# Kernel optimization log

Measured on AMD Instinct MI355X. Metric: run time of the kernel, lower is better.

Reference implementation:

```python
import jax, jax.numpy as jnp
import numpy as np

B, D = 8, 256
MEM, CW, R, K, KL = 131072, 64, 4, 4, 4
C = R * K + 2 * KL + 1  # 25 visible cells
DELTA = 0.005
EPS = 1e-6
TIMESTEP = 1.0  # first step after reset


def _gather(x, idx):
    # x: (b,m) or (b,m,w); idx: (b,k)
    if x.ndim == 2:
        return jnp.take_along_axis(x, idx, axis=1)
    e = jnp.broadcast_to(idx[:, :, None], idx.shape + (x.shape[-1],))
    return jnp.take_along_axis(x, e, axis=1)


def _fwd(xi, memory, visible_memory, link_matrix, rev_link_matrix, precedence,
         read_weights, write_weights, usage,
         W_rq, b_rq, W_wv, b_wv, W_ig, b_ig, W_wg, b_wg,
         read_positions):
    b = xi.shape[0]
    bidx = jnp.arange(b)[:, None]

    # interface transforms (independent linears)
    read_query = (xi @ W_rq + b_rq).reshape(b, R, CW)      # (b,r,w)
    write_vector = (xi @ W_wv + b_wv).reshape(b, 1, CW)    # (b,1,w)
    ig = jax.nn.sigmoid(xi @ W_ig + b_ig)                  # (b,c)
    wg = jax.nn.sigmoid(xi @ W_wg + b_wg)                  # (b,1)

    # ------------------ write ------------------
    rw_vis = _gather(read_weights, read_positions)         # (b,c)
    ww_vis = _gather(write_weights, read_positions)        # (b,c)

    # usage update + least-used indicator over visible cells
    u = (rw_vis + ww_vis > DELTA).astype(memory.dtype)
    rel = _gather(usage, read_positions)
    I_min = (rel == jnp.min(rel, axis=-1, keepdims=True)).astype(memory.dtype)
    rel_new = (TIMESTEP - rel) * u + rel * (1.0 - u)
    usage = usage.at[bidx, read_positions].set(rel_new)

    # interpolated write weights over visible cells
    ww_new = wg * (ig * rw_vis + (1.0 - ig) * I_min)       # (b,c)
    write_weights = write_weights.at[bidx, read_positions].set(ww_new)

    # erase + write into visible memory, scatter back into sparse memory
    visible_memory = visible_memory * (1.0 - I_min[:, :, None]) + ww_new[:, :, None] * write_vector
    memory = memory.at[bidx, read_positions].set(visible_memory)

    # link matrix / reverse link matrix update
    trp = read_positions[:, R * K:R * K + 2 * KL]          # temporal positions (b,2KL)
    Ieye = jnp.eye(MEM, 2 * KL, dtype=memory.dtype)[None]  # eye(m,k) mask as in torch code
    prec_dense = jnp.zeros_like(write_weights).at[bidx, trp].set(precedence)  # (b,m)
    tww = _gather(write_weights, trp)                      # (b,2KL)
    link_matrix = ((1.0 - write_weights[:, :, None]) * link_matrix
                   + write_weights[:, :, None] * precedence[:, None, :]) * Ieye
    rev_link_matrix = ((1.0 - tww[:, None, :]) * rev_link_matrix
                       + tww[:, None, :] * prec_dense[:, :, None]) * Ieye

    # precedence update and least-used cell (argmin usage)
    precedence = (1.0 - jnp.sum(tww, axis=-1, keepdims=True)) * precedence + tww
    least_used = jax.lax.top_k(-usage, 1)[1]               # (b,1)

    # ------------------ read ------------------
    trw = _gather(read_weights, trp)                       # (b,2KL)
    fwd_w = jnp.einsum('bmk,bk->bm', link_matrix, trw)     # forward weighting
    bwd_w = jnp.einsum('bmk,bk->bm', rev_link_matrix, trw) # backward weighting

    # exact L2 k-NN over full memory (dense surrogate for the FAISS search)
    mem_sq = jnp.sum(memory * memory, axis=-1)             # (b,m)
    dots = jnp.einsum('brw,bmw->brm', read_query, memory)  # (b,r,m)
    knn = jax.lax.top_k(2.0 * dots - mem_sq[:, None, :], K)[1].reshape(b, R * K)

    fp = jax.lax.top_k(fwd_w, KL)[1]
    bp = jax.lax.top_k(bwd_w, KL)[1]
    lum = jnp.full((b, 1), C + 1, dtype=knn.dtype)         # timestep <= mem_size branch
    max_length = least_used[0, 0]                          # mem_limit_reached == False
    positions = jnp.clip(
        jnp.concatenate([knn, fp.astype(knn.dtype), bp.astype(knn.dtype), lum], axis=1),
        0, max_length)                                     # (b,c)

    visible = _gather(memory, positions)                   # (b,c,w)
    kq = read_query / (jnp.linalg.norm(read_query, axis=-1, keepdims=True) + EPS)
    vn = visible / (jnp.linalg.norm(visible, axis=-1, keepdims=True) + EPS)
    sim = jnp.einsum('brw,bcw->brc', kq, vn)               # cosine similarity
    rw_c = jax.nn.softmax(sim, axis=-1)                    # (b,r,c)
    read_vectors = jnp.einsum('brc,bcw->brw', rw_c, visible)
    return read_vectors


def setup_inputs() -> dict:
    key = jax.random.key(0)
    ks = jax.random.split(key, 16)
    inp = {}
    inp['xi'] = jax.random.normal(ks[0], (B, D), jnp.float32)
    inp['memory'] = jax.random.normal(ks[1], (B, MEM, CW), jnp.float32)
    inp['visible_memory'] = jax.random.normal(ks[2], (B, C, CW), jnp.float32)
    inp['link_matrix'] = 0.1 * jax.random.uniform(ks[3], (B, MEM, 2 * KL), jnp.float32)
    inp['rev_link_matrix'] = 0.1 * jax.random.uniform(ks[4], (B, MEM, 2 * KL), jnp.float32)
    inp['precedence'] = 0.1 * jax.random.uniform(ks[5], (B, 2 * KL), jnp.float32)
    inp['read_weights'] = 0.01 * jax.random.uniform(ks[6], (B, MEM), jnp.float32)
    inp['write_weights'] = 0.01 * jax.random.uniform(ks[7], (B, MEM), jnp.float32)
    usage = 0.5 + 0.5 * jax.random.uniform(ks[8], (B, MEM), jnp.float32)
    inp['usage'] = usage.at[:, MEM - 1].set(0.0)  # argmin lands at m-1 so the clamp is a no-op
    inp['least_used_mem'] = jnp.full((B, 1), MEM // 2, jnp.int32)
    inp['read_positions'] = jax.random.randint(ks[9], (B, C), 0, MEM)

    def lin(k, fi, fo):
        s = (6.0 / fi) ** 0.5  # kaiming-uniform-like
        return jax.random.uniform(k, (fi, fo), jnp.float32, -s, s)
    inp['W_rq'] = lin(ks[10], D, R * CW); inp['b_rq'] = jnp.zeros((R * CW,), jnp.float32)
    inp['W_wv'] = lin(ks[11], D, CW);     inp['b_wv'] = jnp.zeros((CW,), jnp.float32)
    inp['W_ig'] = lin(ks[12], D, C);      inp['b_ig'] = jnp.zeros((C,), jnp.float32)
    inp['W_wg'] = lin(ks[13], D, 1);      inp['b_wg'] = jnp.zeros((1,), jnp.float32)
    return inp


def reference(xi, memory, visible_memory, link_matrix, rev_link_matrix, precedence,
              read_weights, write_weights, usage, least_used_mem, read_positions,
              W_rq, b_rq, W_wv, b_wv, W_ig, b_ig, W_wg, b_wg):
    # least_used_mem is overwritten inside write() (argmin of updated usage) before use
    return _fwd(xi, memory, visible_memory, link_matrix, rev_link_matrix, precedence,
                read_weights, write_weights, usage,
                W_rq, b_rq, W_wv, b_wv, W_ig, b_ig, W_wg, b_wg,
                read_positions)
```

## Files before the change

### kernel.cpp

```cpp
#include <hip/hip_runtime.h>
#include <math.h>

#define BN 8
#define DDIM 256
#define MEMN 131072
#define CWN 64
#define RN 4
#define CN 25
#define DELTA_C 0.005f
#define EPS_C 1e-6f
#define RPB 1024
#define NBLK (MEMN / RPB)
#define NEG_INF (-3.402823466e38f)
#define IMAX 0x7fffffff
#define UPD_STRIDE 32


__device__ inline void wave_reduce_max(float& v, int& i, int& t) {
#pragma unroll
  for (int off = 32; off; off >>= 1) {
    float ov = __shfl_down(v, off);
    int oi = __shfl_down(i, off);
    int ot = __shfl_down(t, off);
    if (ov > v || (ov == v && oi < i)) { v = ov; i = oi; t = ot; }
  }
}

__device__ inline void block_argmax256(int tid, float v, int i, int t,
                                       float& rv, int& ri, int& rt) {
  __shared__ float sv[4];
  __shared__ int si[4], st[4];
  __shared__ float bv;
  __shared__ int bi, bt;
  wave_reduce_max(v, i, t);
  if ((tid & 63) == 0) { int w = tid >> 6; sv[w] = v; si[w] = i; st[w] = t; }
  __syncthreads();
  if (tid == 0) {
    float xv = sv[0]; int xi = si[0], xt = st[0];
#pragma unroll
    for (int w = 1; w < 4; w++)
      if (sv[w] > xv || (sv[w] == xv && si[w] < xi)) { xv = sv[w]; xi = si[w]; xt = st[w]; }
    bv = xv; bi = xi; bt = xt;
  }
  __syncthreads();
  rv = bv; ri = bi; rt = bt;
  __syncthreads();
}

__device__ inline void top4_of8(const float* v8, int* out4) {
  float val[12]; int idx[12]; bool used[12];
#pragma unroll
  for (int i = 0; i < 12; i++) { val[i] = (i < 8) ? v8[i] : 0.f; idx[i] = i; used[i] = false; }
  for (int r = 0; r < 4; r++) {
    int best = -1;
    for (int i = 0; i < 12; i++) {
      if (used[i]) continue;
      if (best < 0 || val[i] > val[best]) best = i;
    }
    used[best] = true;
    out4[r] = idx[best];
  }
}

__global__ __launch_bounds__(256) void k1_heads(
    const float* __restrict__ xi,
    const float* __restrict__ Wrq, const float* __restrict__ brq,
    const float* __restrict__ Wwv, const float* __restrict__ bwv,
    const float* __restrict__ Wig, const float* __restrict__ big,
    const float* __restrict__ Wwg, const float* __restrict__ bwg,
    float* rq, float* wv, float* ig, float* wg) {
  int b = blockIdx.x, tid = threadIdx.x;
  __shared__ float x[DDIM];
  x[tid] = xi[b * DDIM + tid];
  __syncthreads();
  {
    float s = brq[tid];
#pragma unroll 8
    for (int d = 0; d < DDIM; d++) s = fmaf(x[d], Wrq[d * 256 + tid], s);
    rq[b * 256 + tid] = s;
  }
  if (tid < 64) {
    float s = bwv[tid];
#pragma unroll 8
    for (int d = 0; d < DDIM; d++) s = fmaf(x[d], Wwv[d * 64 + tid], s);
    wv[b * 64 + tid] = s;
  } else if (tid < 64 + CN) {
    int o = tid - 64;
    float s = big[o];
#pragma unroll 8
    for (int d = 0; d < DDIM; d++) s = fmaf(x[d], Wig[d * CN + o], s);
    ig[b * CN + o] = 1.f / (1.f + expf(-s));
  } else if (tid == 64 + CN) {
    float s = bwg[0];
#pragma unroll 8
    for (int d = 0; d < DDIM; d++) s = fmaf(x[d], Wwg[d], s);
    wg[b] = 1.f / (1.f + expf(-s));
  }
}

__global__ __launch_bounds__(256) void k2_state(
    const float* __restrict__ vm, const float* __restrict__ prec,
    const float* __restrict__ rw, const float* __restrict__ wwg,
    const float* __restrict__ usage,
    const float* __restrict__ lm, const float* __restrict__ rlm,
    const int* __restrict__ rp,
    const float* __restrict__ wv, const float* __restrict__ ig,
    const float* __restrict__ wg, int* fp, int* bp,
    int* upd_pos, float* upd_rel, float* upd_mem) {
  int b = blockIdx.x, tid = threadIdx.x;
  __shared__ int pos[CN];
  __shared__ float s_rw[CN], s_ww[CN], s_rel[CN], s_relnew[CN], s_imin[CN], s_wwnew[CN];
  __shared__ int s_guard[CN];
  __shared__ float minrel;
  __shared__ float fwd8[8], bwd8[8];

  if (tid < CN) {
    int p = rp[b * CN + tid];
    pos[tid] = p;
    s_rw[tid] = rw[(size_t)b * MEMN + p];
    s_ww[tid] = wwg[(size_t)b * MEMN + p];
    s_rel[tid] = usage[(size_t)b * MEMN + p];
  }
  __syncthreads();
  if (tid == 0) {
    float m = s_rel[0];
    for (int j = 1; j < CN; j++) m = fminf(m, s_rel[j]);
    minrel = m;
  }
  __syncthreads();
  if (tid < CN) {
    float u = (s_rw[tid] + s_ww[tid] > DELTA_C) ? 1.f : 0.f;
    float im = (s_rel[tid] == minrel) ? 1.f : 0.f;
    s_imin[tid] = im;
    s_relnew[tid] = u * (1.f - s_rel[tid]) + (1.f - u) * s_rel[tid];
    float igv = ig[b * CN + tid];
    s_wwnew[tid] = wg[b] * (igv * s_rw[tid] + (1.f - igv) * im);
    int g = 1;
    for (int j = tid + 1; j < CN; j++)
      if (pos[j] == pos[tid]) { g = 0; break; }
    s_guard[tid] = g;
  }
  __syncthreads();
  if (tid < CN) {
    upd_pos[b * UPD_STRIDE + tid] = s_guard[tid] ? pos[tid] : -1;
    upd_rel[b * UPD_STRIDE + tid] = s_relnew[tid];
  }
  for (int it = 0; it < 7; it++) {
    int j = it * 4 + (tid >> 6);
    int lane = tid & 63;
    if (j < CN && s_guard[j]) {
      float v = vm[((size_t)b * CN + j) * 64 + lane] * (1.f - s_imin[j]) +
                s_wwnew[j] * wv[b * 64 + lane];
      upd_mem[((size_t)b * CN + j) * 64 + lane] = v;
    }
  }
  __syncthreads();
  if (tid < 8) {
    int m = tid;
    int trp_m = pos[16 + m];
    float tww = 0.f;
    for (int j = CN - 1; j >= 0; j--)
      if (pos[j] == trp_m) { tww = s_wwnew[j]; break; }
    float trw = rw[(size_t)b * MEMN + trp_m];
    float wwu;
    {
      int found = -1;
      for (int j = CN - 1; j >= 0; j--)
        if (pos[j] == m) { found = j; break; }
      wwu = (found >= 0) ? s_wwnew[found] : wwg[(size_t)b * MEMN + m];
    }
    float lmd = (1.f - wwu) * lm[((size_t)b * MEMN + m) * 8 + m] + wwu * prec[b * 8 + m];
    float pd = 0.f;
    for (int k = 7; k >= 0; k--)
      if (pos[16 + k] == m) { pd = prec[b * 8 + k]; break; }
    float rld = (1.f - tww) * rlm[((size_t)b * MEMN + m) * 8 + m] + tww * pd;
    fwd8[m] = lmd * trw;
    bwd8[m] = rld * trw;
  }
  __syncthreads();
  if (tid == 0) top4_of8(fwd8, &fp[b * 4]);
  if (tid == 1) top4_of8(bwd8, &bp[b * 4]);
}

__global__ __launch_bounds__(256) void k3_scan(
    const float* __restrict__ memory, const float* __restrict__ usage,
    const float* __restrict__ rq,
    const int* __restrict__ upd_pos, const float* __restrict__ upd_rel,
    const float* __restrict__ upd_mem,
    float* blk_sv, int* blk_si, float* blk_uv, int* blk_ui) {
  int tid = threadIdx.x;
  int b = blockIdx.x / NBLK;
  int blk = blockIdx.x % NBLK;
  int base = blk * RPB;
  int wave = tid >> 6, lane = tid & 63;
  int sub = lane & 15;
  int grp = lane >> 4;

  __shared__ int s_lcnt;
  __shared__ int s_lpos[CN], s_lj[CN];
  __shared__ float s_lrel[CN];
  if (tid == 0) s_lcnt = 0;
  __syncthreads();
  if (tid < CN) {
    int p = upd_pos[b * UPD_STRIDE + tid];
    if (p >= base && p < base + RPB) {
      int k = atomicAdd(&s_lcnt, 1);
      s_lpos[k] = p;
      s_lj[k] = tid;
      s_lrel[k] = upd_rel[b * UPD_STRIDE + tid];
    }
  }
  __syncthreads();
  int lcnt = s_lcnt;
  const float4* upd4 = (const float4*)upd_mem;

  const float4* q4 = (const float4*)(rq + b * 256);
  float4 qf0 = q4[0 * 16 + sub];
  float4 qf1 = q4[1 * 16 + sub];
  float4 qf2 = q4[2 * 16 + sub];
  float4 qf3 = q4[3 * 16 + sub];

  float tv0 = NEG_INF, tv1 = NEG_INF, tv2 = NEG_INF, tv3 = NEG_INF;
  int ti0 = IMAX, ti1 = IMAX, ti2 = IMAX, ti3 = IMAX;

  int rowbase = base + wave * 256;
  const float4* mp = (const float4*)memory;
  size_t lanebase = ((size_t)b * MEMN + rowbase) * 16 + (size_t)grp * 16 + sub;

#pragma unroll 4
  for (int it = 0; it < 64; it++) {
    int m = rowbase + it * 4 + grp;
    float4 x = mp[lanebase + (size_t)it * 64];
    if (lcnt) {
      for (int k = 0; k < lcnt; k++)
        if (m == s_lpos[k])
          x = upd4[((size_t)b * CN + s_lj[k]) * 16 + sub];
    }
    float d0 = fmaf(x.x, qf0.x, fmaf(x.y, qf0.y, fmaf(x.z, qf0.z, x.w * qf0.w)));
    float d1 = fmaf(x.x, qf1.x, fmaf(x.y, qf1.y, fmaf(x.z, qf1.z, x.w * qf1.w)));
    float d2 = fmaf(x.x, qf2.x, fmaf(x.y, qf2.y, fmaf(x.z, qf2.z, x.w * qf2.w)));
    float d3 = fmaf(x.x, qf3.x, fmaf(x.y, qf3.y, fmaf(x.z, qf3.z, x.w * qf3.w)));
    float sq = fmaf(x.x, x.x, fmaf(x.y, x.y, fmaf(x.z, x.z, x.w * x.w)));
#pragma unroll
    for (int off = 1; off < 16; off <<= 1) {
      d0 += __shfl_xor(d0, off);
      d1 += __shfl_xor(d1, off);
      d2 += __shfl_xor(d2, off);
      d3 += __shfl_xor(d3, off);
      sq += __shfl_xor(sq, off);
    }
    float d = (sub == 0) ? d0 : (sub == 1) ? d1 : (sub == 2) ? d2 : d3;
    float s = 2.f * d - sq;
    if (sub < 4) {
      if (s > tv3) {
        tv3 = s; ti3 = m;
        if (tv3 > tv2) { float t = tv2; tv2 = tv3; tv3 = t; int u = ti2; ti2 = ti3; ti3 = u; }
        if (tv2 > tv1) { float t = tv1; tv1 = tv2; tv2 = t; int u = ti1; ti1 = ti2; ti2 = u; }
        if (tv1 > tv0) { float t = tv0; tv0 = tv1; tv1 = t; int u = ti0; ti0 = ti1; ti1 = u; }
      }
    }
  }

  __shared__ float lsv[4][16][4];
  __shared__ int lsi[4][16][4];
  if (sub < 4) {
    int slot = wave * 4 + grp;
    lsv[sub][slot][0] = tv0; lsi[sub][slot][0] = ti0;
    lsv[sub][slot][1] = tv1; lsi[sub][slot][1] = ti1;
    lsv[sub][slot][2] = tv2; lsi[sub][slot][2] = ti2;
    lsv[sub][slot][3] = tv3; lsi[sub][slot][3] = ti3;
  }
  __syncthreads();
  if (tid < 4) {
    int r = tid;
    size_t o = (((size_t)b * 4 + r) * NBLK + blk) * 4;
    for (int round = 0; round < 4; round++) {
      float bv = NEG_INF; int bi = IMAX; int bslot = 0, bj = 0;
      for (int e = 0; e < 64; e++) {
        int sl = e >> 2, j = e & 3;
        float v = lsv[r][sl][j];
        int ix = lsi[r][sl][j];
        if (v > bv || (v == bv && ix < bi)) { bv = v; bi = ix; bslot = sl; bj = j; }
      }
      lsv[r][bslot][bj] = NEG_INF;
      blk_sv[o + round] = bv;
      blk_si[o + round] = bi;
    }
  }

  {
    const float4* u4 = (const float4*)(usage + (size_t)b * MEMN + base);
    float4 uu = u4[tid];
    int mb = base + tid * 4;
    if (lcnt) {
      for (int k = 0; k < lcnt; k++) {
        int d = s_lpos[k] - mb;
        if ((unsigned)d < 4u) {
          float rv = s_lrel[k];
          if (d == 0) uu.x = rv;
          else if (d == 1) uu.y = rv;
          else if (d == 2) uu.z = rv;
          else uu.w = rv;
        }
      }
    }
    float uv = uu.x; int uix = mb;
    if (uu.y < uv) { uv = uu.y; uix = mb + 1; }
    if (uu.z < uv) { uv = uu.z; uix = mb + 2; }
    if (uu.w < uv) { uv = uu.w; uix = mb + 3; }
    float rvv; int rii, rtt;
    block_argmax256(tid, -uv, uix, tid, rvv, rii, rtt);
    if (tid == 0) {
      blk_uv[b * NBLK + blk] = -rvv;
      blk_ui[b * NBLK + blk] = rii;
    }
  }
}

__global__ __launch_bounds__(256) void k4_merge(
    const float* __restrict__ blk_sv, const int* __restrict__ blk_si,
    const float* __restrict__ blk_uv, const int* __restrict__ blk_ui,
    int* knn, int* least) {
  int b = blockIdx.x, tid = threadIdx.x;
  for (int r = 0; r < 4; r++) {
    size_t o = (size_t)(b * 4 + r) * NBLK * 4;
    float v0 = blk_sv[o + 2 * tid], v1 = blk_sv[o + 2 * tid + 1];
    int i0 = blk_si[o + 2 * tid], i1 = blk_si[o + 2 * tid + 1];
    if (v1 > v0 || (v1 == v0 && i1 < i0)) {
      float tv = v0; v0 = v1; v1 = tv;
      int ti = i0; i0 = i1; i1 = ti;
    }
    for (int round = 0; round < 4; round++) {
      float rvv; int rii, rtt;
      block_argmax256(tid, v0, i0, tid, rvv, rii, rtt);
      if (tid == 0) knn[b * 16 + r * 4 + round] = rii;
      if (tid == rtt) { v0 = v1; i0 = i1; v1 = NEG_INF; i1 = IMAX; }
    }
  }
  float uv = (tid < NBLK) ? -blk_uv[b * NBLK + tid] : NEG_INF;
  int uidx = (tid < NBLK) ? blk_ui[b * NBLK + tid] : IMAX;
  float rvv; int rii, rtt;
  block_argmax256(tid, uv, uidx, tid, rvv, rii, rtt);
  if (tid == 0) least[b] = rii;
}

__global__ __launch_bounds__(256) void k5_attn(
    const float* __restrict__ memory, const float* __restrict__ rq,
    const int* __restrict__ knn, const int* __restrict__ fp,
    const int* __restrict__ bp, const int* __restrict__ least,
    const int* __restrict__ upd_pos, const float* __restrict__ upd_mem,
    float* out) {
  int b = blockIdx.x, tid = threadIdx.x;
  __shared__ int pos[CN];
  __shared__ int supd[CN];
  __shared__ int ovr[CN];
  __shared__ float vis[CN][64];
  __shared__ float vnorm[CN];
  __shared__ float rnorm[4];
  __shared__ float sim[4][CN];
  __shared__ float pw[4][CN];
  __shared__ float qs[4][64];
  int L = least[0];
  if (tid < CN) {
    supd[tid] = upd_pos[b * UPD_STRIDE + tid];
    int v;
    if (tid < 16) v = knn[b * 16 + tid];
    else if (tid < 20) v = fp[b * 4 + tid - 16];
    else if (tid < 24) v = bp[b * 4 + tid - 20];
    else v = CN + 1;
    v = min(v, L);
    v = max(v, 0);
    pos[tid] = v;
  }
  qs[tid >> 6][tid & 63] = rq[b * 256 + tid];
  __syncthreads();
  if (tid < CN) {
    int o = -1;
    for (int j = 0; j < CN; j++)
      if (supd[j] == pos[tid]) o = j;
    ovr[tid] = o;
  }
  __syncthreads();
  for (int it = 0; it < 7; it++) {
    int j = it * 4 + (tid >> 6);
    int lane = tid & 63;
    if (j < CN) {
      int o = ovr[j];
      vis[j][lane] = (o >= 0)
          ? upd_mem[((size_t)b * CN + o) * 64 + lane]
          : memory[((size_t)b * MEMN + pos[j]) * 64 + lane];
    }
  }
  __syncthreads();
  if (tid < CN) {
    float s = 0.f;
    for (int k = 0; k < 64; k++) s = fmaf(vis[tid][k], vis[tid][k], s);
    vnorm[tid] = sqrtf(s) + EPS_C;
  }
  if (tid >= 32 && tid < 36) {
    int r = tid - 32;
    float s = 0.f;
    for (int k = 0; k < 64; k++) s = fmaf(qs[r][k], qs[r][k], s);
    rnorm[r] = sqrtf(s) + EPS_C;
  }
  __syncthreads();
  if (tid < 4 * CN) {
    int r = tid / CN, c = tid % CN;
    float s = 0.f;
    for (int k = 0; k < 64; k++) s = fmaf(qs[r][k], vis[c][k], s);
    sim[r][c] = s / (rnorm[r] * vnorm[c]);
  }
  __syncthreads();
  if (tid < 4) {
    int r = tid;
    float mx = NEG_INF;
    for (int c = 0; c < CN; c++) mx = fmaxf(mx, sim[r][c]);
    float sum = 0.f;
    for (int c = 0; c < CN; c++) { float e = expf(sim[r][c] - mx); pw[r][c] = e; sum += e; }
    float inv = 1.f / sum;
    for (int c = 0; c < CN; c++) pw[r][c] *= inv;
  }
  __syncthreads();
  {
    int r = tid >> 6, w = tid & 63;
    float s = 0.f;
    for (int c = 0; c < CN; c++) s = fmaf(pw[r][c], vis[c][w], s);
    out[(size_t)b * 256 + tid] = s;
  }
}

extern "C" void kernel_launch(void* const* d_in, const int* in_sizes, int n_in,
                              void* d_out, int out_size, void* d_ws, size_t ws_size,
                              hipStream_t stream) {
  const float* xi = (const float*)d_in[0];
  const float* memory = (const float*)d_in[1];
  const float* vm = (const float*)d_in[2];
  const float* lm = (const float*)d_in[3];
  const float* rlm = (const float*)d_in[4];
  const float* prec = (const float*)d_in[5];
  const float* rw = (const float*)d_in[6];
  const float* wwg = (const float*)d_in[7];
  const float* usage = (const float*)d_in[8];
  const int* rp = (const int*)d_in[10];
  const float* Wrq = (const float*)d_in[11];
  const float* brq = (const float*)d_in[12];
  const float* Wwv = (const float*)d_in[13];
  const float* bwv = (const float*)d_in[14];
  const float* Wig = (const float*)d_in[15];
  const float* big = (const float*)d_in[16];
  const float* Wwg = (const float*)d_in[17];
  const float* bwg = (const float*)d_in[18];
  float* out = (float*)d_out;

  float* f = (float*)d_ws;
  float* rq_w = f;      f += BN * 256;
  float* wv_w = f;      f += BN * 64;
  float* upd_mem_w = f; f += (size_t)BN * CN * 64;
  float* ig_w = f;      f += BN * CN;
  float* wg_w = f;      f += BN;
  float* upd_rel_w = f; f += BN * UPD_STRIDE;
  float* blk_sv = f;    f += (size_t)BN * 4 * NBLK * 4;
  float* blk_uv = f;    f += BN * NBLK;
  int* ip = (int*)f;
  int* upd_pos_w = ip;  ip += BN * UPD_STRIDE;
  int* fp_w = ip;       ip += BN * 4;
  int* bp_w = ip;       ip += BN * 4;
  int* knn_w = ip;      ip += BN * 16;
  int* least_w = ip;    ip += BN;
  int* blk_si = ip;     ip += (size_t)BN * 4 * NBLK * 4;
  int* blk_ui = ip;     ip += BN * NBLK;

  hipLaunchKernelGGL(k1_heads, dim3(BN), dim3(256), 0, stream,
                     xi, Wrq, brq, Wwv, bwv, Wig, big, Wwg, bwg,
                     rq_w, wv_w, ig_w, wg_w);
  hipLaunchKernelGGL(k2_state, dim3(BN), dim3(256), 0, stream,
                     vm, prec, rw, wwg, usage, lm, rlm, rp,
                     wv_w, ig_w, wg_w, fp_w, bp_w,
                     upd_pos_w, upd_rel_w, upd_mem_w);
  hipLaunchKernelGGL(k3_scan, dim3(BN * NBLK), dim3(256), 0, stream,
                     memory, usage, rq_w, upd_pos_w, upd_rel_w, upd_mem_w,
                     blk_sv, blk_si, blk_uv, blk_ui);
  hipLaunchKernelGGL(k4_merge, dim3(BN), dim3(256), 0, stream,
                     blk_sv, blk_si, blk_uv, blk_ui, knn_w, least_w);
  hipLaunchKernelGGL(k5_attn, dim3(BN), dim3(256), 0, stream,
                     memory, rq_w, knn_w, fp_w, bp_w, least_w,
                     upd_pos_w, upd_mem_w, out);
}
```

Measured before the change: 526.5 us.

## Fuse head/state and merge/attention kernels, wave-parallel block top-4, usage scan for batch 0

Merges the interface-linear kernel into the state-update kernel, keeping wv, ig and wg in shared memory instead of a global round trip. It also merges the top-k/least-used merge kernel into the attention kernel, using per-wave shuffle reductions. Inside the scan kernel, the serial single-thread top-4 merge per read head is replaced by wave-wide shuffle argmax rounds. The usage argmin is now computed only for batch 0, since only least[0] is consumed downstream. Together these remove two launches and some serial work, at the cost of more shared memory per block and redundant per-batch merge work in the fused kernel.

```diff
diff --git a/kernel.cpp b/kernel.cpp
--- a/kernel.cpp
+++ b/kernel.cpp
@@ -62,15 +62,28 @@
   }
 }
 
-__global__ __launch_bounds__(256) void k1_heads(
+__global__ __launch_bounds__(256) void k12_heads_state(
     const float* __restrict__ xi,
     const float* __restrict__ Wrq, const float* __restrict__ brq,
     const float* __restrict__ Wwv, const float* __restrict__ bwv,
     const float* __restrict__ Wig, const float* __restrict__ big,
     const float* __restrict__ Wwg, const float* __restrict__ bwg,
-    float* rq, float* wv, float* ig, float* wg) {
+    const float* __restrict__ vm, const float* __restrict__ prec,
+    const float* __restrict__ rw, const float* __restrict__ wwg,
+    const float* __restrict__ usage,
+    const float* __restrict__ lm, const float* __restrict__ rlm,
+    const int* __restrict__ rp,
+    float* rq, int* fp, int* bp,
+    int* upd_pos, float* upd_rel, float* upd_mem) {
   int b = blockIdx.x, tid = threadIdx.x;
   __shared__ float x[DDIM];
+  __shared__ float wv_s[64], ig_s[CN], wg_s;
+  __shared__ int pos[CN];
+  __shared__ float s_rw[CN], s_ww[CN], s_rel[CN], s_relnew[CN], s_imin[CN], s_wwnew[CN];
+  __shared__ int s_guard[CN];
+  __shared__ float minrel;
+  __shared__ float fwd8[8], bwd8[8];
+
   x[tid] = xi[b * DDIM + tid];
   __syncthreads();
   {
@@ -83,37 +96,19 @@
     float s = bwv[tid];
 #pragma unroll 8
     for (int d = 0; d < DDIM; d++) s = fmaf(x[d], Wwv[d * 64 + tid], s);
-    wv[b * 64 + tid] = s;
+    wv_s[tid] = s;
   } else if (tid < 64 + CN) {
     int o = tid - 64;
     float s = big[o];
 #pragma unroll 8
     for (int d = 0; d < DDIM; d++) s = fmaf(x[d], Wig[d * CN + o], s);
-    ig[b * CN + o] = 1.f / (1.f + expf(-s));
+    ig_s[o] = 1.f / (1.f + expf(-s));
   } else if (tid == 64 + CN) {
     float s = bwg[0];
 #pragma unroll 8
     for (int d = 0; d < DDIM; d++) s = fmaf(x[d], Wwg[d], s);
-    wg[b] = 1.f / (1.f + expf(-s));
-  }
-}
-
-__global__ __launch_bounds__(256) void k2_state(
-    const float* __restrict__ vm, const float* __restrict__ prec,
-    const float* __restrict__ rw, const float* __restrict__ wwg,
-    const float* __restrict__ usage,
-    const float* __restrict__ lm, const float* __restrict__ rlm,
-    const int* __restrict__ rp,
-    const float* __restrict__ wv, const float* __restrict__ ig,
-    const float* __restrict__ wg, int* fp, int* bp,
-    int* upd_pos, float* upd_rel, float* upd_mem) {
-  int b = blockIdx.x, tid = threadIdx.x;
-  __shared__ int pos[CN];
-  __shared__ float s_rw[CN], s_ww[CN], s_rel[CN], s_relnew[CN], s_imin[CN], s_wwnew[CN];
-  __shared__ int s_guard[CN];
-  __shared__ float minrel;
-  __shared__ float fwd8[8], bwd8[8];
-
+    wg_s = 1.f / (1.f + expf(-s));
+  }
   if (tid < CN) {
     int p = rp[b * CN + tid];
     pos[tid] = p;
@@ -133,8 +128,8 @@
     float im = (s_rel[tid] == minrel) ? 1.f : 0.f;
     s_imin[tid] = im;
     s_relnew[tid] = u * (1.f - s_rel[tid]) + (1.f - u) * s_rel[tid];
-    float igv = ig[b * CN + tid];
-    s_wwnew[tid] = wg[b] * (igv * s_rw[tid] + (1.f - igv) * im);
+    float igv = ig_s[tid];
+    s_wwnew[tid] = wg_s * (igv * s_rw[tid] + (1.f - igv) * im);
     int g = 1;
     for (int j = tid + 1; j < CN; j++)
       if (pos[j] == pos[tid]) { g = 0; break; }
@@ -150,7 +145,7 @@
     int lane = tid & 63;
     if (j < CN && s_guard[j]) {
       float v = vm[((size_t)b * CN + j) * 64 + lane] * (1.f - s_imin[j]) +
-                s_wwnew[j] * wv[b * 64 + lane];
+                s_wwnew[j] * wv_s[lane];
       upd_mem[((size_t)b * CN + j) * 64 + lane] = v;
     }
   }
@@ -271,25 +266,22 @@
     lsv[sub][slot][3] = tv3; lsi[sub][slot][3] = ti3;
   }
   __syncthreads();
-  if (tid < 4) {
-    int r = tid;
-    size_t o = (((size_t)b * 4 + r) * NBLK + blk) * 4;
+  {
+    int w = wave;
+    float v = lsv[w][lane >> 2][lane & 3];
+    int i = lsi[w][lane >> 2][lane & 3];
+    size_t o = (((size_t)b * 4 + w) * NBLK + blk) * 4;
     for (int round = 0; round < 4; round++) {
-      float bv = NEG_INF; int bi = IMAX; int bslot = 0, bj = 0;
-      for (int e = 0; e < 64; e++) {
-        int sl = e >> 2, j = e & 3;
-        float v = lsv[r][sl][j];
-        int ix = lsi[r][sl][j];
-        if (v > bv || (v == bv && ix < bi)) { bv = v; bi = ix; bslot = sl; bj = j; }
-      }
-      lsv[r][bslot][bj] = NEG_INF;
-      blk_sv[o + round] = bv;
-      blk_si[o + round] = bi;
-    }
-  }
-
-  {
-    const float4* u4 = (const float4*)(usage + (size_t)b * MEMN + base);
+      float rv = v; int ri = i; int rt = lane;
+      wave_reduce_max(rv, ri, rt);
+      rv = __shfl(rv, 0); ri = __shfl(ri, 0); rt = __shfl(rt, 0);
+      if (lane == 0) { blk_sv[o + round] = rv; blk_si[o + round] = ri; }
+      if (lane == rt) { v = NEG_INF; i = IMAX; }
+    }
+  }
+
+  if (b == 0) {
+    const float4* u4 = (const float4*)(usage + base);
     float4 uu = u4[tid];
     int mb = base + tid * 4;
     if (lcnt) {
@@ -311,46 +303,23 @@
     float rvv; int rii, rtt;
     block_argmax256(tid, -uv, uix, tid, rvv, rii, rtt);
     if (tid == 0) {
-      blk_uv[b * NBLK + blk] = -rvv;
-      blk_ui[b * NBLK + blk] = rii;
-    }
-  }
-}
-
-__global__ __launch_bounds__(256) void k4_merge(
+      blk_uv[blk] = -rvv;
+      blk_ui[blk] = rii;
+    }
+  }
+}
+
+__global__ __launch_bounds__(256) void k45_merge_attn(
+    const float* __restrict__ memory, const float* __restrict__ rq,
     const float* __restrict__ blk_sv, const int* __restrict__ blk_si,
     const float* __restrict__ blk_uv, const int* __restrict__ blk_ui,
-    int* knn, int* least) {
-  int b = blockIdx.x, tid = threadIdx.x;
-  for (int r = 0; r < 4; r++) {
-    size_t o = (size_t)(b * 4 + r) * NBLK * 4;
-    float v0 = blk_sv[o + 2 * tid], v1 = blk_sv[o + 2 * tid + 1];
-    int i0 = blk_si[o + 2 * tid], i1 = blk_si[o + 2 * tid + 1];
-    if (v1 > v0 || (v1 == v0 && i1 < i0)) {
-      float tv = v0; v0 = v1; v1 = tv;
-      int ti = i0; i0 = i1; i1 = ti;
-    }
-    for (int round = 0; round < 4; round++) {
-      float rvv; int rii, rtt;
-      block_argmax256(tid, v0, i0, tid, rvv, rii, rtt);
-      if (tid == 0) knn[b * 16 + r * 4 + round] = rii;
-      if (tid == rtt) { v0 = v1; i0 = i1; v1 = NEG_INF; i1 = IMAX; }
-    }
-  }
-  float uv = (tid < NBLK) ? -blk_uv[b * NBLK + tid] : NEG_INF;
-  int uidx = (tid < NBLK) ? blk_ui[b * NBLK + tid] : IMAX;
-  float rvv; int rii, rtt;
-  block_argmax256(tid, uv, uidx, tid, rvv, rii, rtt);
-  if (tid == 0) least[b] = rii;
-}
-
-__global__ __launch_bounds__(256) void k5_attn(
-    const float* __restrict__ memory, const float* __restrict__ rq,
-    const int* __restrict__ knn, const int* __restrict__ fp,
-    const int* __restrict__ bp, const int* __restrict__ least,
+    const int* __restrict__ fp, const int* __restrict__ bp,
     const int* __restrict__ upd_pos, const float* __restrict__ upd_mem,
     float* out) {
   int b = blockIdx.x, tid = threadIdx.x;
+  int wave = tid >> 6, lane = tid & 63;
+  __shared__ int knn_s[16];
+  __shared__ int sL;
   __shared__ int pos[CN];
   __shared__ int supd[CN];
   __shared__ int ovr[CN];
@@ -360,11 +329,51 @@
   __shared__ float sim[4][CN];
   __shared__ float pw[4][CN];
   __shared__ float qs[4][64];
-  int L = least[0];
+
+  {
+    int r = wave;
+    size_t o = (size_t)(b * 4 + r) * NBLK * 4;
+    float tv0 = NEG_INF, tv1 = NEG_INF, tv2 = NEG_INF, tv3 = NEG_INF;
+    int ti0 = IMAX, ti1 = IMAX, ti2 = IMAX, ti3 = IMAX;
+#pragma unroll
+    for (int j = 0; j < 8; j++) {
+      float s = blk_sv[o + j * 64 + lane];
+      int m = blk_si[o + j * 64 + lane];
+      if (s > tv3) {
+        tv3 = s; ti3 = m;
+        if (tv3 > tv2) { float t = tv2; tv2 = tv3; tv3 = t; int u = ti2; ti2 = ti3; ti3 = u; }
+        if (tv2 > tv1) { float t = tv1; tv1 = tv2; tv2 = t; int u = ti1; ti1 = ti2; ti2 = u; }
+        if (tv1 > tv0) { float t = tv0; tv0 = tv1; tv1 = t; int u = ti0; ti0 = ti1; ti1 = u; }
+      }
+    }
+    for (int round = 0; round < 4; round++) {
+      float rv = tv0; int ri = ti0; int rt = lane;
+      wave_reduce_max(rv, ri, rt);
+      rv = __shfl(rv, 0); ri = __shfl(ri, 0); rt = __shfl(rt, 0);
+      if (lane == 0) knn_s[r * 4 + round] = ri;
+      if (lane == rt) {
+        tv0 = tv1; ti0 = ti1; tv1 = tv2; ti1 = ti2;
+        tv2 = tv3; ti2 = ti3; tv3 = NEG_INF; ti3 = IMAX;
+      }
+    }
+  }
+  if (wave == 0) {
+    float u0 = blk_uv[lane], u1 = blk_uv[64 + lane];
+    int i0 = blk_ui[lane], i1 = blk_ui[64 + lane];
+    float v; int i;
+    if (u1 < u0 || (u1 == u0 && i1 < i0)) { v = u1; i = i1; } else { v = u0; i = i0; }
+    float rv = -v; int ri = i; int rt = lane;
+    wave_reduce_max(rv, ri, rt);
+    if (lane == 0) sL = ri;
+  }
+  qs[tid >> 6][tid & 63] = rq[b * 256 + tid];
+  __syncthreads();
+
+  int L = sL;
   if (tid < CN) {
     supd[tid] = upd_pos[b * UPD_STRIDE + tid];
     int v;
-    if (tid < 16) v = knn[b * 16 + tid];
+    if (tid < 16) v = knn_s[tid];
     else if (tid < 20) v = fp[b * 4 + tid - 16];
     else if (tid < 24) v = bp[b * 4 + tid - 20];
     else v = CN + 1;
@@ -372,7 +381,6 @@
     v = max(v, 0);
     pos[tid] = v;
   }
-  qs[tid >> 6][tid & 63] = rq[b * 256 + tid];
   __syncthreads();
   if (tid < CN) {
     int o = -1;
@@ -383,12 +391,12 @@
   __syncthreads();
   for (int it = 0; it < 7; it++) {
     int j = it * 4 + (tid >> 6);
-    int lane = tid & 63;
+    int ln = tid & 63;
     if (j < CN) {
       int o = ovr[j];
-      vis[j][lane] = (o >= 0)
-          ? upd_mem[((size_t)b * CN + o) * 64 + lane]
-          : memory[((size_t)b * MEMN + pos[j]) * 64 + lane];
+      vis[j][ln] = (o >= 0)
+          ? upd_mem[((size_t)b * CN + o) * 64 + ln]
+          : memory[((size_t)b * MEMN + pos[j]) * 64 + ln];
     }
   }
   __syncthreads();
@@ -454,35 +462,25 @@
 
   float* f = (float*)d_ws;
   float* rq_w = f;      f += BN * 256;
-  float* wv_w = f;      f += BN * 64;
   float* upd_mem_w = f; f += (size_t)BN * CN * 64;
-  float* ig_w = f;      f += BN * CN;
-  float* wg_w = f;      f += BN;
   float* upd_rel_w = f; f += BN * UPD_STRIDE;
   float* blk_sv = f;    f += (size_t)BN * 4 * NBLK * 4;
-  float* blk_uv = f;    f += BN * NBLK;
+  float* blk_uv = f;    f += NBLK;
   int* ip = (int*)f;
   int* upd_pos_w = ip;  ip += BN * UPD_STRIDE;
   int* fp_w = ip;       ip += BN * 4;
   int* bp_w = ip;       ip += BN * 4;
-  int* knn_w = ip;      ip += BN * 16;
-  int* least_w = ip;    ip += BN;
   int* blk_si = ip;     ip += (size_t)BN * 4 * NBLK * 4;
-  int* blk_ui = ip;     ip += BN * NBLK;
-
-  hipLaunchKernelGGL(k1_heads, dim3(BN), dim3(256), 0, stream,
+  int* blk_ui = ip;     ip += NBLK;
+
+  hipLaunchKernelGGL(k12_heads_state, dim3(BN), dim3(256), 0, stream,
                      xi, Wrq, brq, Wwv, bwv, Wig, big, Wwg, bwg,
-                     rq_w, wv_w, ig_w, wg_w);
-  hipLaunchKernelGGL(k2_state, dim3(BN), dim3(256), 0, stream,
                      vm, prec, rw, wwg, usage, lm, rlm, rp,
-                     wv_w, ig_w, wg_w, fp_w, bp_w,
-                     upd_pos_w, upd_rel_w, upd_mem_w);
+                     rq_w, fp_w, bp_w, upd_pos_w, upd_rel_w, upd_mem_w);
   hipLaunchKernelGGL(k3_scan, dim3(BN * NBLK), dim3(256), 0, stream,
                      memory, usage, rq_w, upd_pos_w, upd_rel_w, upd_mem_w,
                      blk_sv, blk_si, blk_uv, blk_ui);
-  hipLaunchKernelGGL(k4_merge, dim3(BN), dim3(256), 0, stream,
-                     blk_sv, blk_si, blk_uv, blk_ui, knn_w, least_w);
-  hipLaunchKernelGGL(k5_attn, dim3(BN), dim3(256), 0, stream,
-                     memory, rq_w, knn_w, fp_w, bp_w, least_w,
-                     upd_pos_w, upd_mem_w, out);
-}
+  hipLaunchKernelGGL(k45_merge_attn, dim3(BN), dim3(256), 0, stream,
+                     memory, rq_w, blk_sv, blk_si, blk_uv, blk_ui,
+                     fp_w, bp_w, upd_pos_w, upd_mem_w, out);
+}
```

New measurement: 495.0 us. 1.06x faster.
